# Kernel tuning notes

Hardware: AMD Instinct MI355X
Metric: run time of the kernel (lower is better)

Reference implementation:

```python
import jax, jax.numpy as jnp
import numpy as np

D_MODEL = 1024
NUM_HEADS = 16
THETA = 10000.0


def _trunc_normal(key, shape):
    # matches torch.nn.init.trunc_normal_(std=std, a=-3*std, b=3*std)
    std = (2.0 / (shape[0] + shape[1])) ** 0.5
    return jax.random.truncated_normal(key, -3.0, 3.0, shape, dtype=jnp.float32) * std


def setup_inputs() -> dict:
    key = jax.random.key(0)
    kx, kq, kk, kv, ko = jax.random.split(key, 5)
    B, S, D = 2, 2048, D_MODEL
    return {
        "x": jax.random.normal(kx, (B, S, D), dtype=jnp.float32),
        "Wq": _trunc_normal(kq, (D, D)),  # torch Linear weight: [out, in]
        "Wk": _trunc_normal(kk, (D, D)),
        "Wv": _trunc_normal(kv, (D, D)),
        "Wo": _trunc_normal(ko, (D, D)),
        "token_positions": jnp.arange(S, dtype=jnp.int32),
    }


def _rope(x, token_positions):
    # x: [B, H, S, d_k]; RoPE on interleaved pairs (k r) with r=2
    d_k = x.shape[-1]
    inv_freq = THETA ** (-2.0 * jnp.arange(d_k // 2, dtype=jnp.float32) / d_k)
    ang = token_positions.astype(jnp.float32)[:, None] * inv_freq[None, :]  # [S, d_k/2]
    sin, cos = jnp.sin(ang).astype(x.dtype), jnp.cos(ang).astype(x.dtype)
    x0, x1 = x[..., 0::2], x[..., 1::2]
    y0 = x0 * cos - x1 * sin
    y1 = x0 * sin + x1 * cos
    return jnp.stack([y0, y1], axis=-1).reshape(x.shape)


def reference(x, Wq, Wk, Wv, Wo, token_positions):
    B, S, D = x.shape
    H = NUM_HEADS
    d_k = D // H

    def proj(W):  # y = x @ W^T, split heads -> [B, H, S, d_k]
        y = jnp.einsum('bsd,ed->bse', x, W)
        return y.reshape(B, S, H, d_k).transpose(0, 2, 1, 3)

    q = _rope(proj(Wq), token_positions)
    k = _rope(proj(Wk), token_positions)
    v = proj(Wv)

    # causal mask: attend where pos_k <= pos_q
    mask = token_positions[None, :] <= token_positions[:, None]  # [S_q, S_k]
    logits = jnp.einsum('bhqd,bhkd->bhqk', q, k) / (d_k ** 0.5)
    logits = jnp.where(mask, logits, -jnp.inf)
    scores = jax.nn.softmax(logits, axis=-1)
    attn = jnp.einsum('bhqk,bhkd->bhqd', scores, v)  # [B, H, S, d_k]
    attn = attn.transpose(0, 2, 1, 3).reshape(B, S, D)
    return jnp.einsum('bsd,ed->bse', attn, Wo)
```

## Files before the change

kernel.cpp:

```cpp
#include <hip/hip_runtime.h>
#include <hip/hip_bf16.h>

typedef __attribute__((ext_vector_type(8))) short s16x8;
typedef __attribute__((ext_vector_type(4))) float f32x4;

__device__ __forceinline__ unsigned short f2b(float x) {
  unsigned int u = __float_as_uint(x);
  u = (u + 0x7fffu + ((u >> 16) & 1u)) >> 16;
  return (unsigned short)u;
}

__device__ __forceinline__ unsigned int pkbf(float a, float b) {
  return (unsigned int)f2b(a) | ((unsigned int)f2b(b) << 16);
}

__device__ __forceinline__ float b2f(unsigned short u) {
  return __uint_as_float((unsigned int)u << 16);
}

__device__ __forceinline__ void gl2lds16(const unsigned short* g, unsigned short* lds) {
  __builtin_amdgcn_global_load_lds(
      (const __attribute__((address_space(1))) unsigned int*)g,
      (__attribute__((address_space(3))) unsigned int*)lds, 16, 0, 0);
}

__global__ __launch_bounds__(256) void cast_all(
    const float* __restrict__ x,  const float* __restrict__ Wq,
    const float* __restrict__ Wk, const float* __restrict__ Wv,
    const float* __restrict__ Wo, unsigned short* __restrict__ dst) {
  int i = blockIdx.x * 256 + threadIdx.x;
  const float* src;
  int off;
  if (i < 1048576) { src = x; off = i; }
  else {
    int j = i - 1048576;
    int seg = j >> 18;
    off = j & 262143;
    src = (seg == 0) ? Wq : (seg == 1) ? Wk : (seg == 2) ? Wv : Wo;
  }
  const float4 v = ((const float4*)src)[off];
  ushort4 o;
  o.x = f2b(v.x); o.y = f2b(v.y); o.z = f2b(v.z); o.w = f2b(v.w);
  ((ushort4*)dst)[i] = o;
}

#define KDIM 1024

__global__ __launch_bounds__(256, 4) void gemm_qkv(
    const unsigned short* __restrict__ A,
    const unsigned short* __restrict__ Bt,
    const int* __restrict__ tok,
    unsigned short* __restrict__ Qo,
    unsigned short* __restrict__ Ko,
    unsigned short* __restrict__ Vt) {
  __shared__ unsigned short As[2][128 * 32];
  __shared__ unsigned short Bs[2][128 * 32];
  const int tid = threadIdx.x;
  const int bid = blockIdx.x;
  const int xcd = bid & 7;
  const int loc = bid >> 3;
  const int m0 = (loc / 3) * 128;
  const int n0 = (xcd * 3 + loc % 3) * 128;
  const int w = tid >> 6, lane = tid & 63;
  const int ln = lane & 15, quad = lane >> 4;
  const int wm = (w >> 1) * 64, wn = (w & 1) * 64;

  const int rr = lane >> 2;
  const int gsw = ((lane & 3) ^ ((rr ^ (rr >> 2)) & 3)) * 8;
  const int sr = (ln ^ (ln >> 2)) & 3;

  const f32x4 zero = {0.f, 0.f, 0.f, 0.f};
  f32x4 acc[4][4];
#pragma unroll
  for (int i = 0; i < 4; ++i)
#pragma unroll
    for (int j = 0; j < 4; ++j) acc[i][j] = zero;

#define QKV_STAGE(kb, p)                                                              \
  do {                                                                                \
    int col = (kb) * 32 + gsw;                                                        \
    gl2lds16(A  + (size_t)(m0 + w * 32 + rr) * KDIM + col,      &As[p][(w * 32) * 32]);      \
    gl2lds16(A  + (size_t)(m0 + w * 32 + 16 + rr) * KDIM + col, &As[p][(w * 32 + 16) * 32]); \
    gl2lds16(Bt + (size_t)(n0 + w * 32 + rr) * KDIM + col,      &Bs[p][(w * 32) * 32]);      \
    gl2lds16(Bt + (size_t)(n0 + w * 32 + 16 + rr) * KDIM + col, &Bs[p][(w * 32 + 16) * 32]); \
  } while (0)

  QKV_STAGE(0, 0);
  for (int kb = 0; kb < 32; ++kb) {
    const int p = kb & 1;
    __syncthreads();
    if (kb < 31) QKV_STAGE(kb + 1, p ^ 1);
    s16x8 af[4], bfr[4];
#pragma unroll
    for (int i = 0; i < 4; ++i)
      af[i] = *(const s16x8*)(&As[p][(wm + i * 16 + ln) * 32 + ((quad ^ sr) * 8)]);
#pragma unroll
    for (int j = 0; j < 4; ++j)
      bfr[j] = *(const s16x8*)(&Bs[p][(wn + j * 16 + ln) * 32 + ((quad ^ sr) * 8)]);
#pragma unroll
    for (int i = 0; i < 4; ++i)
#pragma unroll
      for (int j = 0; j < 4; ++j)
        acc[i][j] = __builtin_amdgcn_mfma_f32_16x16x32_bf16(af[i], bfr[j], acc[i][j], 0, 0, 0);
  }
#undef QKV_STAGE

  const bool isV = (n0 >= 2048);
  if (!isV) {
#pragma unroll
    for (int j = 0; j < 4; ++j) {
      int gn = n0 + wn + j * 16 + ln;
      int e = gn & 1023;
      int h = e >> 6, d = e & 63;
      float inv = __expf(-0.2878231366f * (float)(d >> 1));
      unsigned short* dst = (gn < 1024) ? Qo : Ko;
#pragma unroll
      for (int i = 0; i < 4; ++i) {
        int gmb = m0 + wm + i * 16 + quad * 4;
#pragma unroll
        for (int r = 0; r < 4; ++r) {
          float val = acc[i][j][r];
          float part = __shfl_xor(val, 1, 64);
          int m = gmb + r;
          int b = m >> 11, s = m & 2047;
          float ang = (float)s * inv;
          float sn, cs;
          __sincosf(ang, &sn, &cs);
          float x0 = (d & 1) ? part : val;
          float x1 = (d & 1) ? val : part;
          float y = (d & 1) ? (x0 * sn + x1 * cs) : (x0 * cs - x1 * sn);
          dst[(((size_t)b * 16 + h) * 2048 + s) * 64 + d] = f2b(y);
        }
      }
    }
  } else {
    __syncthreads();
    unsigned short* T = &As[0][0] + w * 1120;
    const int b = m0 >> 11;
    const int hrow = ((n0 - 2048) + wn) >> 6;
    const int s0 = (m0 & 2047) + wm;
    const size_t vbase = (size_t)(b * 16 + hrow) * 64;
#pragma unroll
    for (int j = 0; j < 4; ++j) {
#pragma unroll
      for (int i = 0; i < 4; ++i)
#pragma unroll
        for (int r = 0; r < 4; ++r)
          T[ln * 70 + i * 16 + quad * 4 + r] = f2b(acc[i][j][r]);
      __builtin_amdgcn_wave_barrier();
#pragma unroll
      for (int dd = 0; dd < 16; ++dd)
        Vt[(vbase + j * 16 + dd) * 2048 + s0 + lane] = T[dd * 70 + lane];
      __builtin_amdgcn_wave_barrier();
    }
  }
}

__global__ __launch_bounds__(256, 3) void attn_partial(
    const unsigned short* __restrict__ Q,
    const unsigned short* __restrict__ K,
    const unsigned short* __restrict__ Vt,
    unsigned short* __restrict__ Opart,
    float2* __restrict__ ML) {
  __shared__ unsigned short Ks[2][64 * 64];
  __shared__ unsigned short Vs[2][64 * 64];
  __shared__ unsigned short Pt[4][16 * 72];

  const int bid = blockIdx.x;
  const int xcd = bid & 7;
  const int loc = bid >> 3;
  const int bh = xcd * 4 + (loc & 3);
  const int widx = loc >> 2;
  int c, qh;
  if (widx < 28) {
    if (widx < 13)      { c = 0; qh = 3 + widx; }
    else if (widx < 22) { c = 1; qh = 7 + (widx - 13); }
    else if (widx < 27) { c = 2; qh = 11 + (widx - 22); }
    else                { c = 3; qh = 15; }
  } else {
    int s = widx - 28;
    int wt = s >> 2;
    c = s & 3;
    qh = 4 * c + 2 - wt;
  }
  const int kbeg = c * 512;
  const int khi = min(kbeg + 512, qh * 128 + 128);
  const int nit = (khi - kbeg) >> 6;

  const int tid = threadIdx.x;
  const int w = tid >> 6, lane = tid & 63;
  const int ln = lane & 15, quad = lane >> 4;
  const int qb = qh * 128 + w * 32;

  const unsigned short* Qb = Q + (size_t)bh * 2048 * 64;
  const unsigned short* Kb = K + (size_t)bh * 2048 * 64;
  const unsigned short* Vb = Vt + (size_t)bh * 64 * 2048;

  const int srow = w * 16 + (lane >> 3);
  const int sg = (lane & 7) ^ (srow & 7);

#define ATTN_STAGE(k0, p)                                                            \
  do {                                                                               \
    gl2lds16(Kb + (size_t)((k0) + srow) * 64 + sg * 8,       &Ks[p][(w * 16) * 64]);      \
    gl2lds16(Kb + (size_t)((k0) + srow + 8) * 64 + sg * 8,   &Ks[p][(w * 16 + 8) * 64]);  \
    gl2lds16(Vb + (size_t)srow * 2048 + (k0) + sg * 8,       &Vs[p][(w * 16) * 64]);      \
    gl2lds16(Vb + (size_t)(srow + 8) * 2048 + (k0) + sg * 8, &Vs[p][(w * 16 + 8) * 64]);  \
  } while (0)

  s16x8 bq[2][2];
#pragma unroll
  for (int u = 0; u < 2; ++u)
#pragma unroll
    for (int hh = 0; hh < 2; ++hh)
      bq[u][hh] = *(const s16x8*)(&Qb[(size_t)(qb + u * 16 + ln) * 64 + hh * 32 + quad * 8]);

  const f32x4 zero = {0.f, 0.f, 0.f, 0.f};
  f32x4 o[2][4];
#pragma unroll
  for (int u = 0; u < 2; ++u)
#pragma unroll
    for (int j = 0; j < 4; ++j) o[u][j] = zero;
  float m_i[2] = {-3e38f, -3e38f};
  float l_i[2] = {0.f, 0.f};

  const int rdsw = ((ln & 7) * 8);

  ATTN_STAGE(kbeg, 0);
  for (int it = 0; it < nit; ++it) {
    const int p = it & 1;
    const int k0 = kbeg + it * 64;
    __syncthreads();
    if (it + 1 < nit) ATTN_STAGE(k0 + 64, p ^ 1);

    s16x8 ka[4][2];
#pragma unroll
    for (int t = 0; t < 4; ++t)
#pragma unroll
      for (int hh = 0; hh < 2; ++hh)
        ka[t][hh] = *(const s16x8*)(&Ks[p][(t * 16 + ln) * 64 + (((hh * 4 + quad) * 8) ^ rdsw)]);

#pragma unroll
    for (int u = 0; u < 2; ++u) {
      const int q = qb + u * 16 + ln;
      f32x4 st[4];
#pragma unroll
      for (int t = 0; t < 4; ++t) {
        f32x4 s = __builtin_amdgcn_mfma_f32_16x16x32_bf16(ka[t][0], bq[u][0], zero, 0, 0, 0);
        st[t] = __builtin_amdgcn_mfma_f32_16x16x32_bf16(ka[t][1], bq[u][1], s, 0, 0, 0);
      }
      float lm = -3e38f;
#pragma unroll
      for (int t = 0; t < 4; ++t)
#pragma unroll
        for (int r = 0; r < 4; ++r) {
          int kk = k0 + t * 16 + quad * 4 + r;
          float v = st[t][r] * 0.125f;
          v = (kk > q) ? -3e38f : v;
          st[t][r] = v;
          lm = fmaxf(lm, v);
        }
      lm = fmaxf(lm, __shfl_xor(lm, 16, 64));
      lm = fmaxf(lm, __shfl_xor(lm, 32, 64));
      float mn = fmaxf(m_i[u], lm);
      float al = __expf(m_i[u] - mn);
      float rs = 0.f;
#pragma unroll
      for (int t = 0; t < 4; ++t)
#pragma unroll
        for (int r = 0; r < 4; ++r) {
          float pv = __expf(st[t][r] - mn);
          st[t][r] = pv;
          rs += pv;
        }
      rs += __shfl_xor(rs, 16, 64);
      rs += __shfl_xor(rs, 32, 64);
      m_i[u] = mn;
      l_i[u] = l_i[u] * al + rs;
#pragma unroll
      for (int j = 0; j < 4; ++j) o[u][j] *= al;

#pragma unroll
      for (int t = 0; t < 4; ++t) {
        uint2 pv;
        pv.x = pkbf(st[t][0], st[t][1]);
        pv.y = pkbf(st[t][2], st[t][3]);
        *(uint2*)(&Pt[w][ln * 72 + t * 16 + quad * 4]) = pv;
      }
      __builtin_amdgcn_wave_barrier();
#pragma unroll
      for (int hh = 0; hh < 2; ++hh) {
        s16x8 pb = *(const s16x8*)(&Pt[w][ln * 72 + hh * 32 + quad * 8]);
#pragma unroll
        for (int j = 0; j < 4; ++j) {
          s16x8 va = *(const s16x8*)(&Vs[p][(j * 16 + ln) * 64 + (((hh * 4 + quad) * 8) ^ rdsw)]);
          o[u][j] = __builtin_amdgcn_mfma_f32_16x16x32_bf16(va, pb, o[u][j], 0, 0, 0);
        }
      }
      __builtin_amdgcn_wave_barrier();
    }
  }
#undef ATTN_STAGE

#pragma unroll
  for (int u = 0; u < 2; ++u) {
    int s = qb + u * 16 + ln;
    size_t row = ((size_t)bh * 4 + c) * 2048 + s;
    if (quad == 0) ML[row] = make_float2(m_i[u], l_i[u]);
    size_t base = row * 64;
#pragma unroll
    for (int j = 0; j < 4; ++j) {
      ushort4 o4;
      o4.x = f2b(o[u][j][0]);
      o4.y = f2b(o[u][j][1]);
      o4.z = f2b(o[u][j][2]);
      o4.w = f2b(o[u][j][3]);
      *(ushort4*)(&Opart[base + j * 16 + quad * 4]) = o4;
    }
  }
}

__global__ __launch_bounds__(256) void attn_merge(
    const unsigned short* __restrict__ Opart,
    const float2* __restrict__ ML,
    unsigned short* __restrict__ Ao) {
  int idx = blockIdx.x * 256 + threadIdx.x;
  int d0 = (idx & 7) * 8;
  int q  = (idx >> 3) & 2047;
  int bh = idx >> 14;
  int nc = (q >> 9) + 1;

  float m_c[4], l_c[4];
  float M = -3e38f;
  for (int c = 0; c < nc; ++c) {
    float2 ml = ML[((size_t)bh * 4 + c) * 2048 + q];
    m_c[c] = ml.x; l_c[c] = ml.y;
    M = fmaxf(M, ml.x);
  }
  float acc[8] = {0, 0, 0, 0, 0, 0, 0, 0};
  float L = 0.f;
  for (int c = 0; c < nc; ++c) {
    float wc = __expf(m_c[c] - M);
    L += wc * l_c[c];
    const ushort4* p = (const ushort4*)(Opart + (((size_t)bh * 4 + c) * 2048 + q) * 64 + d0);
    ushort4 a = p[0], bvec = p[1];
    acc[0] += wc * b2f(a.x); acc[1] += wc * b2f(a.y);
    acc[2] += wc * b2f(a.z); acc[3] += wc * b2f(a.w);
    acc[4] += wc * b2f(bvec.x); acc[5] += wc * b2f(bvec.y);
    acc[6] += wc * b2f(bvec.z); acc[7] += wc * b2f(bvec.w);
  }
  float invL = 1.0f / L;
  int b = bh >> 4, h = bh & 15;
  unsigned short* dst = Ao + ((size_t)b * 2048 + q) * 1024 + h * 64 + d0;
  ushort4 o0, o1;
  o0.x = f2b(acc[0] * invL); o0.y = f2b(acc[1] * invL);
  o0.z = f2b(acc[2] * invL); o0.w = f2b(acc[3] * invL);
  o1.x = f2b(acc[4] * invL); o1.y = f2b(acc[5] * invL);
  o1.z = f2b(acc[6] * invL); o1.w = f2b(acc[7] * invL);
  ((ushort4*)dst)[0] = o0;
  ((ushort4*)dst)[1] = o1;
}

__global__ __launch_bounds__(256, 3) void gemm_out(
    const unsigned short* __restrict__ A,
    const unsigned short* __restrict__ Bt,
    float* __restrict__ out) {
  __shared__ unsigned short As[128 * 64];
  __shared__ unsigned short Bs[128 * 64];
  const int tid = threadIdx.x;
  const int bid = blockIdx.x;
  const int m0 = (bid >> 3) * 128;
  const int n0 = (bid & 7) * 128;
  const int w = tid >> 6, lane = tid & 63;
  const int ln = lane & 15, quad = lane >> 4;
  const int wm = (w >> 1) * 64, wn = (w & 1) * 64;

  const int srow = w * 32 + (lane >> 3);
  const int sg = (lane & 7) ^ (lane >> 3);
  const int rs = ln & 7;

  const f32x4 zero = {0.f, 0.f, 0.f, 0.f};
  f32x4 acc[4][4];
#pragma unroll
  for (int i = 0; i < 4; ++i)
#pragma unroll
    for (int j = 0; j < 4; ++j) acc[i][j] = zero;

  for (int kb = 0; kb < KDIM / 64; ++kb) {
    __syncthreads();
#pragma unroll
    for (int t = 0; t < 4; ++t) {
      gl2lds16(A  + (size_t)(m0 + srow + t * 8) * KDIM + kb * 64 + sg * 8, &As[(w * 32 + t * 8) * 64]);
      gl2lds16(Bt + (size_t)(n0 + srow + t * 8) * KDIM + kb * 64 + sg * 8, &Bs[(w * 32 + t * 8) * 64]);
    }
    __syncthreads();
#pragma unroll
    for (int ks = 0; ks < 2; ++ks) {
      s16x8 af[4], bfr[4];
#pragma unroll
      for (int i = 0; i < 4; ++i)
        af[i] = *(const s16x8*)(&As[(wm + i * 16 + ln) * 64 + (((ks * 4 + quad) ^ rs) * 8)]);
#pragma unroll
      for (int j = 0; j < 4; ++j)
        bfr[j] = *(const s16x8*)(&Bs[(wn + j * 16 + ln) * 64 + (((ks * 4 + quad) ^ rs) * 8)]);
#pragma unroll
      for (int i = 0; i < 4; ++i)
#pragma unroll
        for (int j = 0; j < 4; ++j)
          acc[i][j] = __builtin_amdgcn_mfma_f32_16x16x32_bf16(af[i], bfr[j], acc[i][j], 0, 0, 0);
    }
  }
#pragma unroll
  for (int i = 0; i < 4; ++i) {
    int gmb = m0 + wm + i * 16 + quad * 4;
#pragma unroll
    for (int j = 0; j < 4; ++j) {
      int gn = n0 + wn + j * 16 + ln;
#pragma unroll
      for (int r = 0; r < 4; ++r)
        out[(size_t)(gmb + r) * 1024 + gn] = acc[i][j][r];
    }
  }
}

extern "C" void kernel_launch(void* const* d_in, const int* in_sizes, int n_in,
                              void* d_out, int out_size, void* d_ws, size_t ws_size,
                              hipStream_t stream) {
  const float* x  = (const float*)d_in[0];
  const float* Wq = (const float*)d_in[1];
  const float* Wk = (const float*)d_in[2];
  const float* Wv = (const float*)d_in[3];
  const float* Wo = (const float*)d_in[4];
  const int* tok  = (const int*)d_in[5];
  float* out = (float*)d_out;

  char* ws = (char*)d_ws;
  unsigned short* xb    = (unsigned short*)(ws);
  unsigned short* Wcat  = (unsigned short*)(ws + (8ull  << 20));
  unsigned short* Wob   = (unsigned short*)(ws + (14ull << 20));
  unsigned short* Qb    = (unsigned short*)(ws + (16ull << 20));
  unsigned short* Kb    = (unsigned short*)(ws + (24ull << 20));
  unsigned short* Vtb   = (unsigned short*)(ws + (32ull << 20));
  unsigned short* Ab    = (unsigned short*)(ws + (40ull << 20));
  unsigned short* Opart = (unsigned short*)(ws + (48ull << 20));
  float2*         ML    = (float2*)        (ws + (80ull << 20));

  cast_all<<<dim3(8192), dim3(256), 0, stream>>>(x, Wq, Wk, Wv, Wo, xb);
  gemm_qkv<<<dim3(768), dim3(256), 0, stream>>>(xb, Wcat, tok, Qb, Kb, Vtb);
  attn_partial<<<dim3(1280), dim3(256), 0, stream>>>(Qb, Kb, Vtb, Opart, ML);
  attn_merge<<<dim3(2048), dim3(256), 0, stream>>>(Opart, ML, Ab);
  gemm_out<<<dim3(256), dim3(256), 0, stream>>>(Ab, Wob, out);
}
```

Before: 191.3 us.

## Fold softmax scale into Q, use exp2, skip masked tiles, table RoPE

Folds the 1/sqrt(d) and log2(e) factors into Q so the attention kernel can use exp2 directly. Skips fully masked causal sub-tiles and applies the mask only on diagonal tiles. Skips the rescale of the running output when the row max does not change. Also precomputes a RoPE sin/cos table in the cast kernel and replaces manual bf16 rounding with packed hardware convert instructions. The packed convert and the table lookups may round or load slightly differently, and the table adds extra memory reads in the QKV epilogue.

Result: slower. 198.5 us (+3.8%).

```diff
diff --git a/kernel.cpp b/kernel.cpp
--- a/kernel.cpp
+++ b/kernel.cpp
@@ -10,13 +10,21 @@
   return (unsigned short)u;
 }
 
-__device__ __forceinline__ unsigned int pkbf(float a, float b) {
-  return (unsigned int)f2b(a) | ((unsigned int)f2b(b) << 16);
-}
-
 __device__ __forceinline__ float b2f(unsigned short u) {
   return __uint_as_float((unsigned int)u << 16);
 }
+
+__device__ __forceinline__ unsigned int cvtpk(float a, float b) {
+  unsigned int r;
+  asm("v_cvt_pk_bf16_f32 %0, %1, %2" : "=v"(r) : "v"(a), "v"(b));
+  return r;
+}
+
+#if __has_builtin(__builtin_amdgcn_exp2f)
+__device__ __forceinline__ float fexp2(float x) { return __builtin_amdgcn_exp2f(x); }
+#else
+__device__ __forceinline__ float fexp2(float x) { return exp2f(x); }
+#endif
 
 __device__ __forceinline__ void gl2lds16(const unsigned short* g, unsigned short* lds) {
   __builtin_amdgcn_global_load_lds(
@@ -24,11 +32,25 @@
       (__attribute__((address_space(3))) unsigned int*)lds, 16, 0, 0);
 }
 
+#define QSCALE 0.18033688011f
+
 __global__ __launch_bounds__(256) void cast_all(
     const float* __restrict__ x,  const float* __restrict__ Wq,
     const float* __restrict__ Wk, const float* __restrict__ Wv,
-    const float* __restrict__ Wo, unsigned short* __restrict__ dst) {
-  int i = blockIdx.x * 256 + threadIdx.x;
+    const float* __restrict__ Wo, unsigned short* __restrict__ dst,
+    float2* __restrict__ tbl) {
+  const int blk = blockIdx.x;
+  if (blk >= 8192) {
+    int idx = (blk - 8192) * 256 + threadIdx.x;
+    int s = idx >> 5, d2 = idx & 31;
+    float inv = __expf(-0.2878231366f * (float)d2);
+    float ang = (float)s * inv;
+    float sn, cs;
+    __sincosf(ang, &sn, &cs);
+    tbl[idx] = make_float2(cs, sn);
+    return;
+  }
+  int i = blk * 256 + threadIdx.x;
   const float* src;
   int off;
   if (i < 1048576) { src = x; off = i; }
@@ -39,9 +61,10 @@
     src = (seg == 0) ? Wq : (seg == 1) ? Wk : (seg == 2) ? Wv : Wo;
   }
   const float4 v = ((const float4*)src)[off];
-  ushort4 o;
-  o.x = f2b(v.x); o.y = f2b(v.y); o.z = f2b(v.z); o.w = f2b(v.w);
-  ((ushort4*)dst)[i] = o;
+  uint2 o;
+  o.x = cvtpk(v.x, v.y);
+  o.y = cvtpk(v.z, v.w);
+  ((uint2*)dst)[i] = o;
 }
 
 #define KDIM 1024
@@ -52,7 +75,8 @@
     const int* __restrict__ tok,
     unsigned short* __restrict__ Qo,
     unsigned short* __restrict__ Ko,
-    unsigned short* __restrict__ Vt) {
+    unsigned short* __restrict__ Vt,
+    const float2* __restrict__ tbl) {
   __shared__ unsigned short As[2][128 * 32];
   __shared__ unsigned short Bs[2][128 * 32];
   const int tid = threadIdx.x;
@@ -107,6 +131,7 @@
 
   const bool isV = (n0 >= 2048);
   if (!isV) {
+    const float qs = (n0 < 1024) ? QSCALE : 1.0f;
 #pragma unroll
     for (int j = 0; j < 4; ++j) {
       int gn = n0 + wn + j * 16 + ln;
@@ -123,13 +148,18 @@
           float part = __shfl_xor(val, 1, 64);
           int m = gmb + r;
           int b = m >> 11, s = m & 2047;
-          float ang = (float)s * inv;
           float sn, cs;
-          __sincosf(ang, &sn, &cs);
+          if (tbl) {
+            float2 t = tbl[(s << 5) + (d >> 1)];
+            cs = t.x; sn = t.y;
+          } else {
+            float ang = (float)s * inv;
+            __sincosf(ang, &sn, &cs);
+          }
           float x0 = (d & 1) ? part : val;
           float x1 = (d & 1) ? val : part;
           float y = (d & 1) ? (x0 * sn + x1 * cs) : (x0 * cs - x1 * sn);
-          dst[(((size_t)b * 16 + h) * 2048 + s) * 64 + d] = f2b(y);
+          dst[(((size_t)b * 16 + h) * 2048 + s) * 64 + d] = f2b(y * qs);
         }
       }
     }
@@ -232,71 +262,98 @@
     __syncthreads();
     if (it + 1 < nit) ATTN_STAGE(k0 + 64, p ^ 1);
 
-    s16x8 ka[4][2];
-#pragma unroll
-    for (int t = 0; t < 4; ++t)
-#pragma unroll
-      for (int hh = 0; hh < 2; ++hh)
-        ka[t][hh] = *(const s16x8*)(&Ks[p][(t * 16 + ln) * 64 + (((hh * 4 + quad) * 8) ^ rdsw)]);
-
-#pragma unroll
-    for (int u = 0; u < 2; ++u) {
-      const int q = qb + u * 16 + ln;
-      f32x4 st[4];
-#pragma unroll
-      for (int t = 0; t < 4; ++t) {
-        f32x4 s = __builtin_amdgcn_mfma_f32_16x16x32_bf16(ka[t][0], bq[u][0], zero, 0, 0, 0);
-        st[t] = __builtin_amdgcn_mfma_f32_16x16x32_bf16(ka[t][1], bq[u][1], s, 0, 0, 0);
+    if (k0 <= qb + 31) {
+      s16x8 ka[4][2];
+#pragma unroll
+      for (int t = 0; t < 4; ++t)
+#pragma unroll
+        for (int hh = 0; hh < 2; ++hh)
+          ka[t][hh] = *(const s16x8*)(&Ks[p][(t * 16 + ln) * 64 + (((hh * 4 + quad) * 8) ^ rdsw)]);
+
+#pragma unroll
+      for (int u = 0; u < 2; ++u) {
+        const int qlo = qb + u * 16;
+        if (k0 > qlo + 15) continue;
+        f32x4 st[4];
+#pragma unroll
+        for (int t = 0; t < 4; ++t) {
+          f32x4 s = __builtin_amdgcn_mfma_f32_16x16x32_bf16(ka[t][0], bq[u][0], zero, 0, 0, 0);
+          st[t] = __builtin_amdgcn_mfma_f32_16x16x32_bf16(ka[t][1], bq[u][1], s, 0, 0, 0);
+        }
+        float lm = -3e38f;
+        if (k0 + 63 > qlo) {
+          const int q = qlo + ln;
+#pragma unroll
+          for (int t = 0; t < 4; ++t)
+#pragma unroll
+            for (int r = 0; r < 4; ++r) {
+              int kk = k0 + t * 16 + quad * 4 + r;
+              float v = st[t][r];
+              v = (kk > q) ? -3e38f : v;
+              st[t][r] = v;
+              lm = fmaxf(lm, v);
+            }
+        } else {
+#pragma unroll
+          for (int t = 0; t < 4; ++t)
+#pragma unroll
+            for (int r = 0; r < 4; ++r) lm = fmaxf(lm, st[t][r]);
+        }
+        lm = fmaxf(lm, __shfl_xor(lm, 16, 64));
+        lm = fmaxf(lm, __shfl_xor(lm, 32, 64));
+
+        float rs = 0.f;
+        if (__all(lm <= m_i[u])) {
+          const float mn = m_i[u];
+#pragma unroll
+          for (int t = 0; t < 4; ++t)
+#pragma unroll
+            for (int r = 0; r < 4; ++r) {
+              float pv = fexp2(st[t][r] - mn);
+              st[t][r] = pv;
+              rs += pv;
+            }
+          rs += __shfl_xor(rs, 16, 64);
+          rs += __shfl_xor(rs, 32, 64);
+          l_i[u] += rs;
+        } else {
+          const float mn = fmaxf(m_i[u], lm);
+          const float al = fexp2(m_i[u] - mn);
+#pragma unroll
+          for (int t = 0; t < 4; ++t)
+#pragma unroll
+            for (int r = 0; r < 4; ++r) {
+              float pv = fexp2(st[t][r] - mn);
+              st[t][r] = pv;
+              rs += pv;
+            }
+          rs += __shfl_xor(rs, 16, 64);
+          rs += __shfl_xor(rs, 32, 64);
+          m_i[u] = mn;
+          l_i[u] = l_i[u] * al + rs;
+#pragma unroll
+          for (int j = 0; j < 4; ++j) o[u][j] *= al;
+        }
+
+#pragma unroll
+        for (int t = 0; t < 4; ++t) {
+          uint2 pv;
+          pv.x = cvtpk(st[t][0], st[t][1]);
+          pv.y = cvtpk(st[t][2], st[t][3]);
+          *(uint2*)(&Pt[w][ln * 72 + t * 16 + quad * 4]) = pv;
+        }
+        __builtin_amdgcn_wave_barrier();
+#pragma unroll
+        for (int hh = 0; hh < 2; ++hh) {
+          s16x8 pb = *(const s16x8*)(&Pt[w][ln * 72 + hh * 32 + quad * 8]);
+#pragma unroll
+          for (int j = 0; j < 4; ++j) {
+            s16x8 va = *(const s16x8*)(&Vs[p][(j * 16 + ln) * 64 + (((hh * 4 + quad) * 8) ^ rdsw)]);
+            o[u][j] = __builtin_amdgcn_mfma_f32_16x16x32_bf16(va, pb, o[u][j], 0, 0, 0);
+          }
+        }
+        __builtin_amdgcn_wave_barrier();
       }
-      float lm = -3e38f;
-#pragma unroll
-      for (int t = 0; t < 4; ++t)
-#pragma unroll
-        for (int r = 0; r < 4; ++r) {
-          int kk = k0 + t * 16 + quad * 4 + r;
-          float v = st[t][r] * 0.125f;
-          v = (kk > q) ? -3e38f : v;
-          st[t][r] = v;
-          lm = fmaxf(lm, v);
-        }
-      lm = fmaxf(lm, __shfl_xor(lm, 16, 64));
-      lm = fmaxf(lm, __shfl_xor(lm, 32, 64));
-      float mn = fmaxf(m_i[u], lm);
-      float al = __expf(m_i[u] - mn);
-      float rs = 0.f;
-#pragma unroll
-      for (int t = 0; t < 4; ++t)
-#pragma unroll
-        for (int r = 0; r < 4; ++r) {
-          float pv = __expf(st[t][r] - mn);
-          st[t][r] = pv;
-          rs += pv;
-        }
-      rs += __shfl_xor(rs, 16, 64);
-      rs += __shfl_xor(rs, 32, 64);
-      m_i[u] = mn;
-      l_i[u] = l_i[u] * al + rs;
-#pragma unroll
-      for (int j = 0; j < 4; ++j) o[u][j] *= al;
-
-#pragma unroll
-      for (int t = 0; t < 4; ++t) {
-        uint2 pv;
-        pv.x = pkbf(st[t][0], st[t][1]);
-        pv.y = pkbf(st[t][2], st[t][3]);
-        *(uint2*)(&Pt[w][ln * 72 + t * 16 + quad * 4]) = pv;
-      }
-      __builtin_amdgcn_wave_barrier();
-#pragma unroll
-      for (int hh = 0; hh < 2; ++hh) {
-        s16x8 pb = *(const s16x8*)(&Pt[w][ln * 72 + hh * 32 + quad * 8]);
-#pragma unroll
-        for (int j = 0; j < 4; ++j) {
-          s16x8 va = *(const s16x8*)(&Vs[p][(j * 16 + ln) * 64 + (((hh * 4 + quad) * 8) ^ rdsw)]);
-          o[u][j] = __builtin_amdgcn_mfma_f32_16x16x32_bf16(va, pb, o[u][j], 0, 0, 0);
-        }
-      }
-      __builtin_amdgcn_wave_barrier();
     }
   }
 #undef ATTN_STAGE
@@ -309,12 +366,10 @@
     size_t base = row * 64;
 #pragma unroll
     for (int j = 0; j < 4; ++j) {
-      ushort4 o4;
-      o4.x = f2b(o[u][j][0]);
-      o4.y = f2b(o[u][j][1]);
-      o4.z = f2b(o[u][j][2]);
-      o4.w = f2b(o[u][j][3]);
-      *(ushort4*)(&Opart[base + j * 16 + quad * 4]) = o4;
+      uint2 o4;
+      o4.x = cvtpk(o[u][j][0], o[u][j][1]);
+      o4.y = cvtpk(o[u][j][2], o[u][j][3]);
+      *(uint2*)(&Opart[base + j * 16 + quad * 4]) = o4;
     }
   }
 }
@@ -339,7 +394,7 @@
   float acc[8] = {0, 0, 0, 0, 0, 0, 0, 0};
   float L = 0.f;
   for (int c = 0; c < nc; ++c) {
-    float wc = __expf(m_c[c] - M);
+    float wc = fexp2(m_c[c] - M);
     L += wc * l_c[c];
     const ushort4* p = (const ushort4*)(Opart + (((size_t)bh * 4 + c) * 2048 + q) * 64 + d0);
     ushort4 a = p[0], bvec = p[1];
@@ -351,13 +406,13 @@
   float invL = 1.0f / L;
   int b = bh >> 4, h = bh & 15;
   unsigned short* dst = Ao + ((size_t)b * 2048 + q) * 1024 + h * 64 + d0;
-  ushort4 o0, o1;
-  o0.x = f2b(acc[0] * invL); o0.y = f2b(acc[1] * invL);
-  o0.z = f2b(acc[2] * invL); o0.w = f2b(acc[3] * invL);
-  o1.x = f2b(acc[4] * invL); o1.y = f2b(acc[5] * invL);
-  o1.z = f2b(acc[6] * invL); o1.w = f2b(acc[7] * invL);
-  ((ushort4*)dst)[0] = o0;
-  ((ushort4*)dst)[1] = o1;
+  uint2 o0, o1;
+  o0.x = cvtpk(acc[0] * invL, acc[1] * invL);
+  o0.y = cvtpk(acc[2] * invL, acc[3] * invL);
+  o1.x = cvtpk(acc[4] * invL, acc[5] * invL);
+  o1.y = cvtpk(acc[6] * invL, acc[7] * invL);
+  ((uint2*)dst)[0] = o0;
+  ((uint2*)dst)[1] = o1;
 }
 
 __global__ __launch_bounds__(256, 3) void gemm_out(
@@ -443,9 +498,12 @@
   unsigned short* Ab    = (unsigned short*)(ws + (40ull << 20));
   unsigned short* Opart = (unsigned short*)(ws + (48ull << 20));
   float2*         ML    = (float2*)        (ws + (80ull << 20));
-
-  cast_all<<<dim3(8192), dim3(256), 0, stream>>>(x, Wq, Wk, Wv, Wo, xb);
-  gemm_qkv<<<dim3(768), dim3(256), 0, stream>>>(xb, Wcat, tok, Qb, Kb, Vtb);
+  float2* tbl = (ws_size >= (82ull << 20) + 65536 * sizeof(float2))
+                    ? (float2*)(ws + (82ull << 20)) : (float2*)0;
+
+  const int castGrid = tbl ? 8448 : 8192;
+  cast_all<<<dim3(castGrid), dim3(256), 0, stream>>>(x, Wq, Wk, Wv, Wo, xb, tbl);
+  gemm_qkv<<<dim3(768), dim3(256), 0, stream>>>(xb, Wcat, tok, Qb, Kb, Vtb, tbl);
   attn_partial<<<dim3(1280), dim3(256), 0, stream>>>(Qb, Kb, Vtb, Opart, ML);
   attn_merge<<<dim3(2048), dim3(256), 0, stream>>>(Opart, ML, Ab);
   gemm_out<<<dim3(256), dim3(256), 0, stream>>>(Ab, Wob, out);
```
